# Kernel tuning notes

Measured on AMD Instinct MI355X. Metric: run time of the kernel, lower is better.

The kernel has to match this reference:

```python
import jax, jax.numpy as jnp
import numpy as np

N_NODES = 100000
N_EDGES = 1000000
KEY_DIM = 128
VAL_DIM = 64


def setup_inputs() -> dict:
    key = jax.random.key(0)
    k0, k1, k2, k3, k4, k5 = jax.random.split(key, 6)
    triples = jax.random.randint(k0, (N_EDGES, 3), 0, N_NODES, dtype=jnp.int64)
    ent_feats = jax.random.normal(k1, (N_NODES, KEY_DIM), dtype=jnp.float32)
    att_feats = jax.random.normal(k2, (N_NODES, KEY_DIM), dtype=jnp.float32)
    val_feats = jax.random.normal(k3, (N_NODES, VAL_DIM), dtype=jnp.float32)
    # a: Linear(2*key_dim, 1) -> weight vector [2k], bias [1]
    a_w = jax.random.normal(k4, (2 * KEY_DIM,), dtype=jnp.float32) * (1.0 / np.sqrt(2 * KEY_DIM))
    a_b = jnp.zeros((1,), dtype=jnp.float32)
    W = jax.random.normal(k5, (KEY_DIM + VAL_DIM, KEY_DIM), dtype=jnp.float32) * (1.0 / np.sqrt(KEY_DIM + VAL_DIM))
    return {"attribute_triples": triples, "ent_feats": ent_feats,
            "att_feats": att_feats, "val_feats": val_feats,
            "a_w": a_w, "a_b": a_b, "W": W}


def reference(attribute_triples, ent_feats, att_feats, val_feats, a_w, a_b, W):
    N = ent_feats.shape[0]
    h = attribute_triples[:, 0]
    att = attribute_triples[:, 1]
    val = attribute_triples[:, 2]
    # edge attention score: a([e_h ; a_att]) -> leaky_relu -> exp
    e_h = ent_feats[h]            # [E, K]
    a_f = att_feats[att]          # [E, K]
    score = jnp.concatenate((e_h, a_f), axis=-1) @ a_w + a_b[0]   # [E]
    score = jnp.exp(jax.nn.leaky_relu(score, negative_slope=0.2))
    # segment softmax denominator per head node
    row_sum = jax.ops.segment_sum(score, h, num_segments=N)       # [N]
    attention_p = score / row_sum[h]                               # [E]
    # projected edge messages, weighted by attention, scattered to nodes
    av = jnp.concatenate((a_f, val_feats[val]), axis=-1) @ W       # [E, K]
    av = av * attention_p[:, None]
    to_feats = jax.ops.segment_sum(av, h, num_segments=N)          # [N, K]
    return jax.nn.elu(to_feats + ent_feats)
```

## Files before the change

kernel.cpp:

```cpp
#include <hip/hip_runtime.h>

#define N_NODES 100000
#define N_EDGES 1000000
#define CAP     40

typedef __attribute__((ext_vector_type(4))) float float4_t;
typedef __attribute__((ext_vector_type(2))) _Float16 half2v;
typedef __attribute__((ext_vector_type(4))) _Float16 half4v;
typedef __attribute__((ext_vector_type(8))) _Float16 half8v;
typedef unsigned long long ull;

__device__ __forceinline__ unsigned short f_to_h(float f) {
    union { float f; unsigned int i; } c; c.f = f;
    unsigned int i = c.i;
    unsigned int e = ((i >> 23) & 0xffu) - 112u;
    unsigned int m = i & 0x7fffffu;
    unsigned int r = (e << 10) | (m >> 13);
    r += (m >> 12) & 1u;
    return (unsigned short)r;
}
__device__ __forceinline__ float h_to_f(unsigned short h) {
    union { unsigned int i; float f; } c;
    c.i = (((unsigned int)(h & 0x7fffu)) << 13) + 0x38000000u;
    return c.f;
}
__device__ __forceinline__ unsigned int packh2(float x, float y) {
    half2v h; h.x = (_Float16)x; h.y = (_Float16)y;
    return __builtin_bit_cast(unsigned int, h);
}
__device__ __forceinline__ int clampi(int x) {
    return x < 0 ? 0 : (x >= N_NODES ? N_NODES - 1 : x);
}

__global__ __launch_bounds__(256)
void k_node_scores(const float* __restrict__ ent,
                   const float* __restrict__ attf,
                   const float* __restrict__ valf,
                   const float* __restrict__ aw,
                   float* __restrict__ s_ent, float* __restrict__ s_att,
                   unsigned short* __restrict__ attb,
                   unsigned short* __restrict__ valb) {
    int node = (int)blockIdx.x * 8 + (int)(threadIdx.x >> 5);
    int l32 = threadIdx.x & 31;
    const float4_t* aw4 = (const float4_t*)aw;
    float4_t we4 = aw4[l32];
    float4_t wa4 = aw4[32 + l32];
    float4_t e4 = ((const float4_t*)ent)[(size_t)node * 32 + l32];
    float4_t a4 = ((const float4_t*)attf)[(size_t)node * 32 + l32];
    float2 v2 = ((const float2*)valf)[(size_t)node * 32 + l32];
    if (attb) {
        uint2 pk; pk.x = packh2(a4.x, a4.y); pk.y = packh2(a4.z, a4.w);
        *(uint2*)(attb + (size_t)node * 128 + l32 * 4) = pk;
        ((unsigned int*)valb)[(size_t)node * 32 + l32] = packh2(v2.x, v2.y);
    }
    float se = e4.x * we4.x + e4.y * we4.y + e4.z * we4.z + e4.w * we4.w;
    float sa = a4.x * wa4.x + a4.y * wa4.y + a4.z * wa4.z + a4.w * wa4.w;
#pragma unroll
    for (int off = 16; off >= 1; off >>= 1) {
        se += __shfl_xor(se, off, 64);
        sa += __shfl_xor(sa, off, 64);
    }
    if (l32 == 0) { s_ent[node] = se; s_att[node] = sa; }
}

__global__ __launch_bounds__(256)
void k_prepW(const float* __restrict__ W, unsigned short* __restrict__ Wt) {
    int i = (int)(blockIdx.x * blockDim.x + threadIdx.x);
    if (i >= 192 * 128) return;
    int c = i / 192, k = i - c * 192;
    Wt[i] = __builtin_bit_cast(unsigned short, (_Float16)W[k * 128 + c]);
}

__global__ __launch_bounds__(256)
void k_place(const int* __restrict__ tri,
             const float* __restrict__ s_ent, const float* __restrict__ s_att,
             const float* __restrict__ abp,
             int* __restrict__ cursor, ull* __restrict__ edges) {
    int t = (int)(blockIdx.x * blockDim.x + threadIdx.x);
    if (t >= N_EDGES / 4) return;
    const int4* t4 = (const int4*)tri;
    int4 w0 = t4[3 * t], w1 = t4[3 * t + 1], w2 = t4[3 * t + 2];
    int hs[4] = {w0.x, w0.w, w1.z, w2.y};
    int as[4] = {w0.y, w1.x, w1.w, w2.z};
    int vs[4] = {w0.z, w1.y, w2.x, w2.w};
    float ab = abp[0];
#pragma unroll
    for (int i = 0; i < 4; ++i) {
        int h = clampi(hs[i]), a = clampi(as[i]), v = clampi(vs[i]);
        float s = s_ent[h] + s_att[a] + ab;
        s = s > 0.f ? s : 0.2f * s;
        float sc = __expf(s);
        int slot = atomicAdd(&cursor[h], 1);
        if (slot < CAP) {
            ull pk = (ull)(unsigned)a | ((ull)(unsigned)v << 17) | ((ull)f_to_h(sc) << 34);
            __builtin_nontemporal_store(pk, edges + (size_t)h * CAP + slot);
        }
    }
}

__global__ __launch_bounds__(256)
void k_fused_h(const int* __restrict__ cursor, const ull* __restrict__ edges,
               const unsigned short* __restrict__ attb, const unsigned short* __restrict__ valb,
               const unsigned short* __restrict__ Wt, const float* __restrict__ ent,
               float* __restrict__ out) {
    __shared__ unsigned short Gl[16][200];
    int w = threadIdx.x >> 6, lane = threadIdx.x & 63;
    int grp = lane >> 4, l = lane & 15;
    int base = (int)blockIdx.x * 16;
    int node = base + w * 4 + grp;
    int src = grp << 4;

    int cnt = cursor[node]; cnt = cnt > CAP ? CAP : cnt;
    size_t beg = (size_t)node * CAP;
    const half8v* ap = (const half8v*)attb;
    const half4v* vp = (const half4v*)valb;

    half8v accA = {};
    half4v accV = {};
    float rsum = 0.f;
    int nbat = (cnt + 15) >> 4;
    for (int b = 0; b < nbat; ++b) {
        int idx = b * 16 + l;
        ull edreg = __builtin_nontemporal_load(edges + beg + (idx < cnt ? idx : 0));
        int lim = cnt - b * 16; lim = lim > 16 ? 16 : lim;
#pragma unroll
        for (int c = 0; c < 4; ++c) {
            int j0 = c * 4;
            if (j0 < lim) {
                bool m1 = j0 + 1 < lim, m2 = j0 + 2 < lim, m3 = j0 + 3 < lim;
                ull e0 = __shfl(edreg, src | j0, 64);
                ull e1 = __shfl(edreg, src | (m1 ? j0 + 1 : 0), 64);
                ull e2 = __shfl(edreg, src | (m2 ? j0 + 2 : 0), 64);
                ull e3 = __shfl(edreg, src | (m3 ? j0 + 3 : 0), 64);
                int a0 = (int)(e0 & 0x1FFFFu), v0 = (int)((e0 >> 17) & 0x1FFFFu);
                int a1 = m1 ? (int)(e1 & 0x1FFFFu) : 0, v1 = m1 ? (int)((e1 >> 17) & 0x1FFFFu) : 0;
                int a2 = m2 ? (int)(e2 & 0x1FFFFu) : 0, v2 = m2 ? (int)((e2 >> 17) & 0x1FFFFu) : 0;
                int a3 = m3 ? (int)(e3 & 0x1FFFFu) : 0, v3 = m3 ? (int)((e3 >> 17) & 0x1FFFFu) : 0;
                _Float16 s0 = __builtin_bit_cast(_Float16, (unsigned short)(e0 >> 34));
                _Float16 s1 = m1 ? __builtin_bit_cast(_Float16, (unsigned short)(e1 >> 34)) : (_Float16)0.f;
                _Float16 s2 = m2 ? __builtin_bit_cast(_Float16, (unsigned short)(e2 >> 34)) : (_Float16)0.f;
                _Float16 s3 = m3 ? __builtin_bit_cast(_Float16, (unsigned short)(e3 >> 34)) : (_Float16)0.f;
                half8v A0 = ap[a0 * 16 + l];
                half4v V0 = vp[v0 * 16 + l];
                half8v A1 = ap[a1 * 16 + l];
                half4v V1 = vp[v1 * 16 + l];
                half8v A2 = ap[a2 * 16 + l];
                half4v V2 = vp[v2 * 16 + l];
                half8v A3 = ap[a3 * 16 + l];
                half4v V3 = vp[v3 * 16 + l];
                rsum += (float)s0 + (float)s1 + (float)s2 + (float)s3;
                accA += A0 * s0; accV += V0 * s0;
                accA += A1 * s1; accV += V1 * s1;
                accA += A2 * s2; accV += V2 * s2;
                accA += A3 * s3; accV += V3 * s3;
            }
        }
    }
    {
        float inv = rsum > 0.f ? 1.f / rsum : 0.f;
        _Float16 ih = (_Float16)inv;
        unsigned short* gp = &Gl[w * 4 + grp][0];
        *(half8v*)(gp + l * 8) = accA * ih;
        *(half4v*)(gp + 128 + l * 4) = accV * ih;
    }
    __syncthreads();

    int quad = grp, mn = l;
    float4_t acc0 = {0.f, 0.f, 0.f, 0.f}, acc1 = {0.f, 0.f, 0.f, 0.f};
#pragma unroll
    for (int kt = 0; kt < 6; ++kt) {
        half8v afr = *(const half8v*)(&Gl[mn][quad * 8 + kt * 32]);
        half8v b0 = *(const half8v*)(Wt + (size_t)((w * 2 + 0) * 16 + mn) * 192 + quad * 8 + kt * 32);
        half8v b1 = *(const half8v*)(Wt + (size_t)((w * 2 + 1) * 16 + mn) * 192 + quad * 8 + kt * 32);
        acc0 = __builtin_amdgcn_mfma_f32_16x16x32_f16(afr, b0, acc0, 0, 0, 0);
        acc1 = __builtin_amdgcn_mfma_f32_16x16x32_f16(afr, b1, acc1, 0, 0, 0);
    }
#pragma unroll
    for (int cti = 0; cti < 2; ++cti) {
        float4_t acc = cti ? acc1 : acc0;
        int col = (w * 2 + cti) * 16 + mn;
#pragma unroll
        for (int r = 0; r < 4; ++r) {
            int nd = base + quad * 4 + r;
            float x = acc[r] + __builtin_nontemporal_load(ent + (size_t)nd * 128 + col);
            __builtin_nontemporal_store(x > 0.f ? x : expm1f(x),
                                        out + (size_t)nd * 128 + col);
        }
    }
}

__global__ __launch_bounds__(256)
void k_fused_f32(const int* __restrict__ cursor, const ull* __restrict__ edges,
                 const float* __restrict__ attf, const float* __restrict__ valf,
                 const unsigned short* __restrict__ Wt, const float* __restrict__ ent,
                 float* __restrict__ out) {
    __shared__ unsigned short Gl[16][200];
    int w = threadIdx.x >> 6, lane = threadIdx.x & 63;
    int grp = lane >> 4, l = lane & 15;
    int base = (int)blockIdx.x * 16;

    for (int nn = 0; nn < 4; ++nn) {
        int node = base + w * 4 + nn;
        int cnt = cursor[node]; if (cnt > CAP) cnt = CAP;
        size_t beg = (size_t)node * CAP;
        float aa[8] = {0.f, 0.f, 0.f, 0.f, 0.f, 0.f, 0.f, 0.f};
        float av[4] = {0.f, 0.f, 0.f, 0.f};
        float rsum = 0.f;
        for (int j = grp; j < cnt; j += 4) {
            ull ed = edges[beg + j];
            int a = (int)(ed & 0x1FFFFu);
            int v = (int)((ed >> 17) & 0x1FFFFu);
            float sc = h_to_f((unsigned short)(ed >> 34));
            rsum += sc;
            const float4_t* ap = (const float4_t*)(attf + (size_t)a * 128);
            float4_t f0 = ap[l], f1 = ap[16 + l];
            float4_t fv = ((const float4_t*)(valf + (size_t)v * 64))[l];
#pragma unroll
            for (int q = 0; q < 4; ++q) {
                aa[q] += sc * f0[q]; aa[4 + q] += sc * f1[q]; av[q] += sc * fv[q];
            }
        }
#pragma unroll
        for (int q = 0; q < 8; ++q) {
            aa[q] += __shfl_xor(aa[q], 16, 64);
            aa[q] += __shfl_xor(aa[q], 32, 64);
        }
#pragma unroll
        for (int q = 0; q < 4; ++q) {
            av[q] += __shfl_xor(av[q], 16, 64);
            av[q] += __shfl_xor(av[q], 32, 64);
        }
        rsum += __shfl_xor(rsum, 16, 64);
        rsum += __shfl_xor(rsum, 32, 64);
        if (grp == 0) {
            float inv = rsum > 0.f ? 1.f / rsum : 0.f;
            unsigned short* gp = &Gl[w * 4 + nn][0];
            uint2 p0; p0.x = packh2(aa[0] * inv, aa[1] * inv); p0.y = packh2(aa[2] * inv, aa[3] * inv);
            *(uint2*)(gp + l * 4) = p0;
            uint2 p1; p1.x = packh2(aa[4] * inv, aa[5] * inv); p1.y = packh2(aa[6] * inv, aa[7] * inv);
            *(uint2*)(gp + 64 + l * 4) = p1;
            uint2 pv; pv.x = packh2(av[0] * inv, av[1] * inv); pv.y = packh2(av[2] * inv, av[3] * inv);
            *(uint2*)(gp + 128 + l * 4) = pv;
        }
    }
    __syncthreads();

    int quad = grp, mn = l;
    float4_t acc0 = {0.f, 0.f, 0.f, 0.f}, acc1 = {0.f, 0.f, 0.f, 0.f};
#pragma unroll
    for (int kt = 0; kt < 6; ++kt) {
        half8v afr = *(const half8v*)(&Gl[mn][quad * 8 + kt * 32]);
        half8v b0 = *(const half8v*)(Wt + (size_t)((w * 2 + 0) * 16 + mn) * 192 + quad * 8 + kt * 32);
        half8v b1 = *(const half8v*)(Wt + (size_t)((w * 2 + 1) * 16 + mn) * 192 + quad * 8 + kt * 32);
        acc0 = __builtin_amdgcn_mfma_f32_16x16x32_f16(afr, b0, acc0, 0, 0, 0);
        acc1 = __builtin_amdgcn_mfma_f32_16x16x32_f16(afr, b1, acc1, 0, 0, 0);
    }
#pragma unroll
    for (int cti = 0; cti < 2; ++cti) {
        float4_t acc = cti ? acc1 : acc0;
        int col = (w * 2 + cti) * 16 + mn;
#pragma unroll
        for (int r = 0; r < 4; ++r) {
            int node = base + quad * 4 + r;
            float x = acc[r] + ent[(size_t)node * 128 + col];
            out[(size_t)node * 128 + col] = x > 0.f ? x : expm1f(x);
        }
    }
}

extern "C" void kernel_launch(void* const* d_in, const int* in_sizes, int n_in,
                              void* d_out, int out_size, void* d_ws, size_t ws_size,
                              hipStream_t stream) {
    const int*   tri  = (const int*)d_in[0];
    const float* ent  = (const float*)d_in[1];
    const float* attf = (const float*)d_in[2];
    const float* valf = (const float*)d_in[3];
    const float* aw   = (const float*)d_in[4];
    const float* ab   = (const float*)d_in[5];
    const float* W    = (const float*)d_in[6];
    float* out = (float*)d_out;

    char* ws = (char*)d_ws;
    size_t off = 0;
    int*   cursor = (int*)(ws + off);   off += (size_t)N_NODES * 4;
    float* s_ent  = (float*)(ws + off); off += (size_t)N_NODES * 4;
    float* s_att  = (float*)(ws + off); off += (size_t)N_NODES * 4;
    unsigned short* Wt = (unsigned short*)(ws + off); off += 192 * 128 * 2;
    ull* edges = (ull*)(ws + off);      off += (size_t)N_NODES * CAP * 8;
    unsigned short* attb = (unsigned short*)(ws + off); off += (size_t)N_NODES * 128 * 2;
    unsigned short* valb = (unsigned short*)(ws + off); off += (size_t)N_NODES * 64 * 2;
    size_t need = off;
    int h16 = ws_size >= need;

    hipMemsetAsync(cursor, 0, (size_t)N_NODES * 4, stream);

    k_node_scores<<<N_NODES / 8, 256, 0, stream>>>(ent, attf, valf, aw, s_ent, s_att,
                                                   h16 ? attb : (unsigned short*)nullptr,
                                                   h16 ? valb : (unsigned short*)nullptr);
    k_prepW<<<(192 * 128 + 255) / 256, 256, 0, stream>>>(W, Wt);
    k_place<<<(N_EDGES / 4 + 255) / 256, 256, 0, stream>>>(tri, s_ent, s_att, ab, cursor, edges);
    if (h16)
        k_fused_h<<<N_NODES / 16, 256, 0, stream>>>(cursor, edges, attb, valb, Wt, ent, out);
    else
        k_fused_f32<<<N_NODES / 16, 256, 0, stream>>>(cursor, edges, attf, valf, Wt, ent, out);
}
```

Before: 328.4 us.

## Fuse all stages into one persistent kernel with grid barriers and dynamic tile scheduling

Replaces the memset plus four kernel launches with a single persistent kernel sized to full occupancy. Software grid barriers separate the node-score, edge-placement and gather/MFMA phases, and an atomic tile counter hands out work in the final phase. This is meant to remove launch gaps and tail effects between stages. In exchange, the grid barriers add spin-wait cost, the persistent grid may reduce latency hiding in the memory-bound phases, and the edge loop now reads the triples with scalar loads instead of int4 loads.

```diff
diff --git a/kernel.cpp b/kernel.cpp
--- a/kernel.cpp
+++ b/kernel.cpp
@@ -3,6 +3,7 @@
 #define N_NODES 100000
 #define N_EDGES 1000000
 #define CAP     40
+#define NTILES  (N_NODES / 16)
 
 typedef __attribute__((ext_vector_type(4))) float float4_t;
 typedef __attribute__((ext_vector_type(2))) _Float16 half2v;
@@ -32,14 +33,183 @@
     return x < 0 ? 0 : (x >= N_NODES ? N_NODES - 1 : x);
 }
 
+__device__ __forceinline__ void grid_barrier(int* cnt, int nblocks) {
+    __syncthreads();
+    if (threadIdx.x == 0) {
+        __threadfence();
+        __hip_atomic_fetch_add(cnt, 1, __ATOMIC_ACQ_REL, __HIP_MEMORY_SCOPE_AGENT);
+        while (__hip_atomic_load(cnt, __ATOMIC_ACQUIRE, __HIP_MEMORY_SCOPE_AGENT) < nblocks)
+            __builtin_amdgcn_s_sleep(2);
+    }
+    __syncthreads();
+}
+
+__global__ __launch_bounds__(256, 8)
+void k_mega(const int* __restrict__ tri, const float* __restrict__ ent,
+            const float* __restrict__ attf, const float* __restrict__ valf,
+            const float* __restrict__ aw, const float* __restrict__ abp,
+            const float* __restrict__ W,
+            int* __restrict__ ctrl,
+            int* __restrict__ cursor, float* __restrict__ s_ent, float* __restrict__ s_att,
+            unsigned short* __restrict__ attb, unsigned short* __restrict__ valb,
+            unsigned short* __restrict__ Wt, ull* __restrict__ edges,
+            float* __restrict__ out) {
+    int tid = threadIdx.x;
+    int gtid = (int)blockIdx.x * 256 + tid;
+    int gsz = (int)gridDim.x * 256;
+    int l32 = tid & 31;
+
+    for (int i = gtid; i < N_NODES; i += gsz) cursor[i] = 0;
+    for (int i = gtid; i < 192 * 128; i += gsz) {
+        int c = i / 192, k = i - c * 192;
+        Wt[i] = __builtin_bit_cast(unsigned short, (_Float16)W[k * 128 + c]);
+    }
+    {
+        const float4_t* aw4 = (const float4_t*)aw;
+        float4_t we4 = aw4[l32];
+        float4_t wa4 = aw4[32 + l32];
+        int halfid = ((int)blockIdx.x << 3) + (tid >> 5);
+        int nstep = (int)gridDim.x << 3;
+        for (int node = halfid; node < N_NODES; node += nstep) {
+            float4_t e4 = ((const float4_t*)ent)[(size_t)node * 32 + l32];
+            float4_t a4 = ((const float4_t*)attf)[(size_t)node * 32 + l32];
+            float se = e4.x * we4.x + e4.y * we4.y + e4.z * we4.z + e4.w * we4.w;
+            float sa = a4.x * wa4.x + a4.y * wa4.y + a4.z * wa4.z + a4.w * wa4.w;
+#pragma unroll
+            for (int off = 16; off >= 1; off >>= 1) {
+                se += __shfl_xor(se, off, 64);
+                sa += __shfl_xor(sa, off, 64);
+            }
+            if (l32 == 0) { s_ent[node] = se; s_att[node] = sa; }
+        }
+    }
+    grid_barrier(&ctrl[0], (int)gridDim.x);
+
+    {
+        int halfid = ((int)blockIdx.x << 3) + (tid >> 5);
+        int nstep = (int)gridDim.x << 3;
+        for (int node = halfid; node < N_NODES; node += nstep) {
+            float4_t a4 = ((const float4_t*)attf)[(size_t)node * 32 + l32];
+            float2 v2 = ((const float2*)valf)[(size_t)node * 32 + l32];
+            uint2 pk; pk.x = packh2(a4.x, a4.y); pk.y = packh2(a4.z, a4.w);
+            *(uint2*)(attb + (size_t)node * 128 + l32 * 4) = pk;
+            ((unsigned int*)valb)[(size_t)node * 32 + l32] = packh2(v2.x, v2.y);
+        }
+        float ab = abp[0];
+        for (int e = gtid; e < N_EDGES; e += gsz) {
+            int h = clampi(tri[3 * e]);
+            int a = clampi(tri[3 * e + 1]);
+            int v = clampi(tri[3 * e + 2]);
+            float s = s_ent[h] + s_att[a] + ab;
+            s = s > 0.f ? s : 0.2f * s;
+            float sc = __expf(s);
+            int slot = atomicAdd(&cursor[h], 1);
+            if (slot < CAP) {
+                ull pk = (ull)(unsigned)a | ((ull)(unsigned)v << 17) | ((ull)f_to_h(sc) << 34);
+                __builtin_nontemporal_store(pk, edges + (size_t)h * CAP + slot);
+            }
+        }
+    }
+    grid_barrier(&ctrl[1], (int)gridDim.x);
+
+    __shared__ unsigned short Gl[16][200];
+    __shared__ int s_tile;
+    int w = tid >> 6, lane = tid & 63;
+    int grp = lane >> 4, l = lane & 15;
+    const half8v* ap = (const half8v*)attb;
+    const half4v* vp = (const half4v*)valb;
+    for (;;) {
+        __syncthreads();
+        if (tid == 0) s_tile = atomicAdd(&ctrl[2], 1);
+        __syncthreads();
+        int tile = s_tile;
+        if (tile >= NTILES) break;
+        int base = tile * 16;
+        int node = base + w * 4 + grp;
+        int src = grp << 4;
+        int cnt = cursor[node]; cnt = cnt > CAP ? CAP : cnt;
+        size_t beg = (size_t)node * CAP;
+
+        half8v accA = {};
+        half4v accV = {};
+        float rsum = 0.f;
+        int nbat = (cnt + 15) >> 4;
+        for (int b = 0; b < nbat; ++b) {
+            int idx = b * 16 + l;
+            ull edreg = __builtin_nontemporal_load(edges + beg + (idx < cnt ? idx : 0));
+            int lim = cnt - b * 16; lim = lim > 16 ? 16 : lim;
+#pragma unroll
+            for (int c = 0; c < 4; ++c) {
+                int j0 = c * 4;
+                if (j0 < lim) {
+                    bool m1 = j0 + 1 < lim, m2 = j0 + 2 < lim, m3 = j0 + 3 < lim;
+                    ull e0 = __shfl(edreg, src | j0, 64);
+                    ull e1 = __shfl(edreg, src | (m1 ? j0 + 1 : 0), 64);
+                    ull e2 = __shfl(edreg, src | (m2 ? j0 + 2 : 0), 64);
+                    ull e3 = __shfl(edreg, src | (m3 ? j0 + 3 : 0), 64);
+                    int a0 = (int)(e0 & 0x1FFFFu), v0 = (int)((e0 >> 17) & 0x1FFFFu);
+                    int a1 = m1 ? (int)(e1 & 0x1FFFFu) : 0, v1 = m1 ? (int)((e1 >> 17) & 0x1FFFFu) : 0;
+                    int a2 = m2 ? (int)(e2 & 0x1FFFFu) : 0, v2 = m2 ? (int)((e2 >> 17) & 0x1FFFFu) : 0;
+                    int a3 = m3 ? (int)(e3 & 0x1FFFFu) : 0, v3 = m3 ? (int)((e3 >> 17) & 0x1FFFFu) : 0;
+                    _Float16 s0 = __builtin_bit_cast(_Float16, (unsigned short)(e0 >> 34));
+                    _Float16 s1 = m1 ? __builtin_bit_cast(_Float16, (unsigned short)(e1 >> 34)) : (_Float16)0.f;
+                    _Float16 s2 = m2 ? __builtin_bit_cast(_Float16, (unsigned short)(e2 >> 34)) : (_Float16)0.f;
+                    _Float16 s3 = m3 ? __builtin_bit_cast(_Float16, (unsigned short)(e3 >> 34)) : (_Float16)0.f;
+                    half8v A0 = ap[a0 * 16 + l];
+                    half4v V0 = vp[v0 * 16 + l];
+                    half8v A1 = ap[a1 * 16 + l];
+                    half4v V1 = vp[v1 * 16 + l];
+                    half8v A2 = ap[a2 * 16 + l];
+                    half4v V2 = vp[v2 * 16 + l];
+                    half8v A3 = ap[a3 * 16 + l];
+                    half4v V3 = vp[v3 * 16 + l];
+                    rsum += (float)s0 + (float)s1 + (float)s2 + (float)s3;
+                    accA += A0 * s0; accV += V0 * s0;
+                    accA += A1 * s1; accV += V1 * s1;
+                    accA += A2 * s2; accV += V2 * s2;
+                    accA += A3 * s3; accV += V3 * s3;
+                }
+            }
+        }
+        {
+            float inv = rsum > 0.f ? 1.f / rsum : 0.f;
+            _Float16 ih = (_Float16)inv;
+            unsigned short* gp = &Gl[w * 4 + grp][0];
+            *(half8v*)(gp + l * 8) = accA * ih;
+            *(half4v*)(gp + 128 + l * 4) = accV * ih;
+        }
+        __syncthreads();
+
+        int quad = grp, mn = l;
+        float4_t acc0 = {0.f, 0.f, 0.f, 0.f}, acc1 = {0.f, 0.f, 0.f, 0.f};
+#pragma unroll
+        for (int kt = 0; kt < 6; ++kt) {
+            half8v afr = *(const half8v*)(&Gl[mn][quad * 8 + kt * 32]);
+            half8v b0 = *(const half8v*)(Wt + (size_t)((w * 2 + 0) * 16 + mn) * 192 + quad * 8 + kt * 32);
+            half8v b1 = *(const half8v*)(Wt + (size_t)((w * 2 + 1) * 16 + mn) * 192 + quad * 8 + kt * 32);
+            acc0 = __builtin_amdgcn_mfma_f32_16x16x32_f16(afr, b0, acc0, 0, 0, 0);
+            acc1 = __builtin_amdgcn_mfma_f32_16x16x32_f16(afr, b1, acc1, 0, 0, 0);
+        }
+#pragma unroll
+        for (int cti = 0; cti < 2; ++cti) {
+            float4_t acc = cti ? acc1 : acc0;
+            int col = (w * 2 + cti) * 16 + mn;
+#pragma unroll
+            for (int r = 0; r < 4; ++r) {
+                int nd = base + quad * 4 + r;
+                float x = acc[r] + __builtin_nontemporal_load(ent + (size_t)nd * 128 + col);
+                __builtin_nontemporal_store(x > 0.f ? x : expm1f(x),
+                                            out + (size_t)nd * 128 + col);
+            }
+        }
+    }
+}
+
 __global__ __launch_bounds__(256)
-void k_node_scores(const float* __restrict__ ent,
-                   const float* __restrict__ attf,
-                   const float* __restrict__ valf,
-                   const float* __restrict__ aw,
+void k_node_scores(const float* __restrict__ ent, const float* __restrict__ attf,
+                   const float* __restrict__ valf, const float* __restrict__ aw,
                    float* __restrict__ s_ent, float* __restrict__ s_att,
-                   unsigned short* __restrict__ attb,
-                   unsigned short* __restrict__ valb) {
+                   unsigned short* __restrict__ attb, unsigned short* __restrict__ valb) {
     int node = (int)blockIdx.x * 8 + (int)(threadIdx.x >> 5);
     int l32 = threadIdx.x & 31;
     const float4_t* aw4 = (const float4_t*)aw;
@@ -72,120 +242,21 @@
 }
 
 __global__ __launch_bounds__(256)
-void k_place(const int* __restrict__ tri,
-             const float* __restrict__ s_ent, const float* __restrict__ s_att,
-             const float* __restrict__ abp,
+void k_place(const int* __restrict__ tri, const float* __restrict__ s_ent,
+             const float* __restrict__ s_att, const float* __restrict__ abp,
              int* __restrict__ cursor, ull* __restrict__ edges) {
-    int t = (int)(blockIdx.x * blockDim.x + threadIdx.x);
-    if (t >= N_EDGES / 4) return;
-    const int4* t4 = (const int4*)tri;
-    int4 w0 = t4[3 * t], w1 = t4[3 * t + 1], w2 = t4[3 * t + 2];
-    int hs[4] = {w0.x, w0.w, w1.z, w2.y};
-    int as[4] = {w0.y, w1.x, w1.w, w2.z};
-    int vs[4] = {w0.z, w1.y, w2.x, w2.w};
-    float ab = abp[0];
-#pragma unroll
-    for (int i = 0; i < 4; ++i) {
-        int h = clampi(hs[i]), a = clampi(as[i]), v = clampi(vs[i]);
-        float s = s_ent[h] + s_att[a] + ab;
-        s = s > 0.f ? s : 0.2f * s;
-        float sc = __expf(s);
-        int slot = atomicAdd(&cursor[h], 1);
-        if (slot < CAP) {
-            ull pk = (ull)(unsigned)a | ((ull)(unsigned)v << 17) | ((ull)f_to_h(sc) << 34);
-            __builtin_nontemporal_store(pk, edges + (size_t)h * CAP + slot);
-        }
-    }
-}
-
-__global__ __launch_bounds__(256)
-void k_fused_h(const int* __restrict__ cursor, const ull* __restrict__ edges,
-               const unsigned short* __restrict__ attb, const unsigned short* __restrict__ valb,
-               const unsigned short* __restrict__ Wt, const float* __restrict__ ent,
-               float* __restrict__ out) {
-    __shared__ unsigned short Gl[16][200];
-    int w = threadIdx.x >> 6, lane = threadIdx.x & 63;
-    int grp = lane >> 4, l = lane & 15;
-    int base = (int)blockIdx.x * 16;
-    int node = base + w * 4 + grp;
-    int src = grp << 4;
-
-    int cnt = cursor[node]; cnt = cnt > CAP ? CAP : cnt;
-    size_t beg = (size_t)node * CAP;
-    const half8v* ap = (const half8v*)attb;
-    const half4v* vp = (const half4v*)valb;
-
-    half8v accA = {};
-    half4v accV = {};
-    float rsum = 0.f;
-    int nbat = (cnt + 15) >> 4;
-    for (int b = 0; b < nbat; ++b) {
-        int idx = b * 16 + l;
-        ull edreg = __builtin_nontemporal_load(edges + beg + (idx < cnt ? idx : 0));
-        int lim = cnt - b * 16; lim = lim > 16 ? 16 : lim;
-#pragma unroll
-        for (int c = 0; c < 4; ++c) {
-            int j0 = c * 4;
-            if (j0 < lim) {
-                bool m1 = j0 + 1 < lim, m2 = j0 + 2 < lim, m3 = j0 + 3 < lim;
-                ull e0 = __shfl(edreg, src | j0, 64);
-                ull e1 = __shfl(edreg, src | (m1 ? j0 + 1 : 0), 64);
-                ull e2 = __shfl(edreg, src | (m2 ? j0 + 2 : 0), 64);
-                ull e3 = __shfl(edreg, src | (m3 ? j0 + 3 : 0), 64);
-                int a0 = (int)(e0 & 0x1FFFFu), v0 = (int)((e0 >> 17) & 0x1FFFFu);
-                int a1 = m1 ? (int)(e1 & 0x1FFFFu) : 0, v1 = m1 ? (int)((e1 >> 17) & 0x1FFFFu) : 0;
-                int a2 = m2 ? (int)(e2 & 0x1FFFFu) : 0, v2 = m2 ? (int)((e2 >> 17) & 0x1FFFFu) : 0;
-                int a3 = m3 ? (int)(e3 & 0x1FFFFu) : 0, v3 = m3 ? (int)((e3 >> 17) & 0x1FFFFu) : 0;
-                _Float16 s0 = __builtin_bit_cast(_Float16, (unsigned short)(e0 >> 34));
-                _Float16 s1 = m1 ? __builtin_bit_cast(_Float16, (unsigned short)(e1 >> 34)) : (_Float16)0.f;
-                _Float16 s2 = m2 ? __builtin_bit_cast(_Float16, (unsigned short)(e2 >> 34)) : (_Float16)0.f;
-                _Float16 s3 = m3 ? __builtin_bit_cast(_Float16, (unsigned short)(e3 >> 34)) : (_Float16)0.f;
-                half8v A0 = ap[a0 * 16 + l];
-                half4v V0 = vp[v0 * 16 + l];
-                half8v A1 = ap[a1 * 16 + l];
-                half4v V1 = vp[v1 * 16 + l];
-                half8v A2 = ap[a2 * 16 + l];
-                half4v V2 = vp[v2 * 16 + l];
-                half8v A3 = ap[a3 * 16 + l];
-                half4v V3 = vp[v3 * 16 + l];
-                rsum += (float)s0 + (float)s1 + (float)s2 + (float)s3;
-                accA += A0 * s0; accV += V0 * s0;
-                accA += A1 * s1; accV += V1 * s1;
-                accA += A2 * s2; accV += V2 * s2;
-                accA += A3 * s3; accV += V3 * s3;
-            }
-        }
-    }
-    {
-        float inv = rsum > 0.f ? 1.f / rsum : 0.f;
-        _Float16 ih = (_Float16)inv;
-        unsigned short* gp = &Gl[w * 4 + grp][0];
-        *(half8v*)(gp + l * 8) = accA * ih;
-        *(half4v*)(gp + 128 + l * 4) = accV * ih;
-    }
-    __syncthreads();
-
-    int quad = grp, mn = l;
-    float4_t acc0 = {0.f, 0.f, 0.f, 0.f}, acc1 = {0.f, 0.f, 0.f, 0.f};
-#pragma unroll
-    for (int kt = 0; kt < 6; ++kt) {
-        half8v afr = *(const half8v*)(&Gl[mn][quad * 8 + kt * 32]);
-        half8v b0 = *(const half8v*)(Wt + (size_t)((w * 2 + 0) * 16 + mn) * 192 + quad * 8 + kt * 32);
-        half8v b1 = *(const half8v*)(Wt + (size_t)((w * 2 + 1) * 16 + mn) * 192 + quad * 8 + kt * 32);
-        acc0 = __builtin_amdgcn_mfma_f32_16x16x32_f16(afr, b0, acc0, 0, 0, 0);
-        acc1 = __builtin_amdgcn_mfma_f32_16x16x32_f16(afr, b1, acc1, 0, 0, 0);
-    }
-#pragma unroll
-    for (int cti = 0; cti < 2; ++cti) {
-        float4_t acc = cti ? acc1 : acc0;
-        int col = (w * 2 + cti) * 16 + mn;
-#pragma unroll
-        for (int r = 0; r < 4; ++r) {
-            int nd = base + quad * 4 + r;
-            float x = acc[r] + __builtin_nontemporal_load(ent + (size_t)nd * 128 + col);
-            __builtin_nontemporal_store(x > 0.f ? x : expm1f(x),
-                                        out + (size_t)nd * 128 + col);
-        }
+    int e = (int)(blockIdx.x * blockDim.x + threadIdx.x);
+    if (e >= N_EDGES) return;
+    int h = clampi(tri[3 * e]);
+    int a = clampi(tri[3 * e + 1]);
+    int v = clampi(tri[3 * e + 2]);
+    float s = s_ent[h] + s_att[a] + abp[0];
+    s = s > 0.f ? s : 0.2f * s;
+    float sc = __expf(s);
+    int slot = atomicAdd(&cursor[h], 1);
+    if (slot < CAP) {
+        ull pk = (ull)(unsigned)a | ((ull)(unsigned)v << 17) | ((ull)f_to_h(sc) << 34);
+        __builtin_nontemporal_store(pk, edges + (size_t)h * CAP + slot);
     }
 }
 
@@ -198,7 +269,6 @@
     int w = threadIdx.x >> 6, lane = threadIdx.x & 63;
     int grp = lane >> 4, l = lane & 15;
     int base = (int)blockIdx.x * 16;
-
     for (int nn = 0; nn < 4; ++nn) {
         int node = base + w * 4 + nn;
         int cnt = cursor[node]; if (cnt > CAP) cnt = CAP;
@@ -244,7 +314,6 @@
         }
     }
     __syncthreads();
-
     int quad = grp, mn = l;
     float4_t acc0 = {0.f, 0.f, 0.f, 0.f}, acc1 = {0.f, 0.f, 0.f, 0.f};
 #pragma unroll
@@ -282,6 +351,7 @@
 
     char* ws = (char*)d_ws;
     size_t off = 0;
+    int*   ctrl   = (int*)(ws + off);   off += 256;
     int*   cursor = (int*)(ws + off);   off += (size_t)N_NODES * 4;
     float* s_ent  = (float*)(ws + off); off += (size_t)N_NODES * 4;
     float* s_att  = (float*)(ws + off); off += (size_t)N_NODES * 4;
@@ -292,15 +362,30 @@
     size_t need = off;
     int h16 = ws_size >= need;
 
-    hipMemsetAsync(cursor, 0, (size_t)N_NODES * 4, stream);
-
-    k_node_scores<<<N_NODES / 8, 256, 0, stream>>>(ent, attf, valf, aw, s_ent, s_att,
-                                                   h16 ? attb : (unsigned short*)nullptr,
-                                                   h16 ? valb : (unsigned short*)nullptr);
-    k_prepW<<<(192 * 128 + 255) / 256, 256, 0, stream>>>(W, Wt);
-    k_place<<<(N_EDGES / 4 + 255) / 256, 256, 0, stream>>>(tri, s_ent, s_att, ab, cursor, edges);
-    if (h16)
-        k_fused_h<<<N_NODES / 16, 256, 0, stream>>>(cursor, edges, attb, valb, Wt, ent, out);
-    else
+    static int s_nb = 0;
+    if (s_nb == 0) {
+        int occ = 0, ncu = 0, dev = 0;
+        if (hipOccupancyMaxActiveBlocksPerMultiprocessor(&occ, k_mega, 256, 0) != hipSuccess || occ <= 0)
+            occ = -1;
+        (void)hipGetDevice(&dev);
+        if (hipDeviceGetAttribute(&ncu, hipDeviceAttributeMultiprocessorCount, dev) != hipSuccess || ncu <= 0)
+            ncu = 256;
+        s_nb = (occ > 0) ? occ * ncu : -1;
+        if (s_nb > 4096) s_nb = 4096;
+    }
+
+    if (h16 && s_nb > 0) {
+        (void)hipMemsetAsync(ctrl, 0, 12, stream);
+        k_mega<<<s_nb, 256, 0, stream>>>(tri, ent, attf, valf, aw, ab, W,
+                                         ctrl, cursor, s_ent, s_att,
+                                         attb, valb, Wt, edges, out);
+    } else {
+        (void)hipMemsetAsync(cursor, 0, (size_t)N_NODES * 4, stream);
+        k_node_scores<<<N_NODES / 8, 256, 0, stream>>>(ent, attf, valf, aw, s_ent, s_att,
+                                                       h16 ? attb : (unsigned short*)nullptr,
+                                                       h16 ? valb : (unsigned short*)nullptr);
+        k_prepW<<<(192 * 128 + 255) / 256, 256, 0, stream>>>(W, Wt);
+        k_place<<<(N_EDGES + 255) / 256, 256, 0, stream>>>(tri, s_ent, s_att, ab, cursor, edges);
         k_fused_f32<<<N_NODES / 16, 256, 0, stream>>>(cursor, edges, attf, valf, Wt, ent, out);
-}
+    }
+}
```

After: 617.0 us. 87.9% more time.

## Merge node-score prep and edge bucketing into one concurrent kernel, compute scores in gather

Applied to the files above, without the earlier changes.

Edge placement no longer depends on node scores: bucketing stores only (att,val) indices, and the fused gather kernel recomputes each edge's attention score from s_ent[node]+s_att[a]. That lets node-score/fp16 conversion, W transpose and edge bucketing run in one persistent kernel, with even and odd blocks doing the two jobs in opposite order so they overlap. Two launches and a dependency barrier go away. The cost is an extra s_att gather plus an exp per edge in the gather kernel, and the fallback path is refactored into separate kernels.

```diff
diff --git a/kernel.cpp b/kernel.cpp
--- a/kernel.cpp
+++ b/kernel.cpp
@@ -3,6 +3,7 @@
 #define N_NODES 100000
 #define N_EDGES 1000000
 #define CAP     40
+#define NPREP   2048
 
 typedef __attribute__((ext_vector_type(4))) float float4_t;
 typedef __attribute__((ext_vector_type(2))) _Float16 half2v;
@@ -33,73 +34,69 @@
 }
 
 __global__ __launch_bounds__(256)
-void k_node_scores(const float* __restrict__ ent,
-                   const float* __restrict__ attf,
-                   const float* __restrict__ valf,
-                   const float* __restrict__ aw,
-                   float* __restrict__ s_ent, float* __restrict__ s_att,
-                   unsigned short* __restrict__ attb,
-                   unsigned short* __restrict__ valb) {
-    int node = (int)blockIdx.x * 8 + (int)(threadIdx.x >> 5);
-    int l32 = threadIdx.x & 31;
-    const float4_t* aw4 = (const float4_t*)aw;
-    float4_t we4 = aw4[l32];
-    float4_t wa4 = aw4[32 + l32];
-    float4_t e4 = ((const float4_t*)ent)[(size_t)node * 32 + l32];
-    float4_t a4 = ((const float4_t*)attf)[(size_t)node * 32 + l32];
-    float2 v2 = ((const float2*)valf)[(size_t)node * 32 + l32];
-    if (attb) {
-        uint2 pk; pk.x = packh2(a4.x, a4.y); pk.y = packh2(a4.z, a4.w);
-        *(uint2*)(attb + (size_t)node * 128 + l32 * 4) = pk;
-        ((unsigned int*)valb)[(size_t)node * 32 + l32] = packh2(v2.x, v2.y);
-    }
-    float se = e4.x * we4.x + e4.y * we4.y + e4.z * we4.z + e4.w * we4.w;
-    float sa = a4.x * wa4.x + a4.y * wa4.y + a4.z * wa4.z + a4.w * wa4.w;
-#pragma unroll
-    for (int off = 16; off >= 1; off >>= 1) {
-        se += __shfl_xor(se, off, 64);
-        sa += __shfl_xor(sa, off, 64);
-    }
-    if (l32 == 0) { s_ent[node] = se; s_att[node] = sa; }
-}
-
-__global__ __launch_bounds__(256)
-void k_prepW(const float* __restrict__ W, unsigned short* __restrict__ Wt) {
-    int i = (int)(blockIdx.x * blockDim.x + threadIdx.x);
-    if (i >= 192 * 128) return;
-    int c = i / 192, k = i - c * 192;
-    Wt[i] = __builtin_bit_cast(unsigned short, (_Float16)W[k * 128 + c]);
-}
-
-__global__ __launch_bounds__(256)
-void k_place(const int* __restrict__ tri,
-             const float* __restrict__ s_ent, const float* __restrict__ s_att,
-             const float* __restrict__ abp,
-             int* __restrict__ cursor, ull* __restrict__ edges) {
-    int t = (int)(blockIdx.x * blockDim.x + threadIdx.x);
-    if (t >= N_EDGES / 4) return;
-    const int4* t4 = (const int4*)tri;
-    int4 w0 = t4[3 * t], w1 = t4[3 * t + 1], w2 = t4[3 * t + 2];
-    int hs[4] = {w0.x, w0.w, w1.z, w2.y};
-    int as[4] = {w0.y, w1.x, w1.w, w2.z};
-    int vs[4] = {w0.z, w1.y, w2.x, w2.w};
-    float ab = abp[0];
-#pragma unroll
-    for (int i = 0; i < 4; ++i) {
-        int h = clampi(hs[i]), a = clampi(as[i]), v = clampi(vs[i]);
-        float s = s_ent[h] + s_att[a] + ab;
-        s = s > 0.f ? s : 0.2f * s;
-        float sc = __expf(s);
-        int slot = atomicAdd(&cursor[h], 1);
-        if (slot < CAP) {
-            ull pk = (ull)(unsigned)a | ((ull)(unsigned)v << 17) | ((ull)f_to_h(sc) << 34);
-            __builtin_nontemporal_store(pk, edges + (size_t)h * CAP + slot);
+void k_prep(const int* __restrict__ tri, const float* __restrict__ ent,
+            const float* __restrict__ attf, const float* __restrict__ valf,
+            const float* __restrict__ aw, const float* __restrict__ W,
+            float* __restrict__ s_ent, float* __restrict__ s_att,
+            unsigned short* __restrict__ attb, unsigned short* __restrict__ valb,
+            unsigned short* __restrict__ Wt,
+            int* __restrict__ cursor, ull* __restrict__ edges) {
+    int bid = (int)blockIdx.x, nbk = (int)gridDim.x, tid = threadIdx.x;
+    bool even = (bid & 1) == 0;
+#pragma unroll
+    for (int pass = 0; pass < 2; ++pass) {
+        if ((pass == 0) == even) {
+            int l32 = tid & 31;
+            const float4_t* aw4 = (const float4_t*)aw;
+            float4_t we4 = aw4[l32];
+            float4_t wa4 = aw4[32 + l32];
+            int halfid = bid * 8 + (tid >> 5);
+            int nstep = nbk * 8;
+            for (int node = halfid; node < N_NODES; node += nstep) {
+                float4_t e4 = ((const float4_t*)ent)[(size_t)node * 32 + l32];
+                float4_t a4 = ((const float4_t*)attf)[(size_t)node * 32 + l32];
+                float2 v2 = ((const float2*)valf)[(size_t)node * 32 + l32];
+                uint2 pk; pk.x = packh2(a4.x, a4.y); pk.y = packh2(a4.z, a4.w);
+                *(uint2*)(attb + (size_t)node * 128 + l32 * 4) = pk;
+                ((unsigned int*)valb)[(size_t)node * 32 + l32] = packh2(v2.x, v2.y);
+                float se = e4.x * we4.x + e4.y * we4.y + e4.z * we4.z + e4.w * we4.w;
+                float sa = a4.x * wa4.x + a4.y * wa4.y + a4.z * wa4.z + a4.w * wa4.w;
+#pragma unroll
+                for (int off = 16; off >= 1; off >>= 1) {
+                    se += __shfl_xor(se, off, 64);
+                    sa += __shfl_xor(sa, off, 64);
+                }
+                if (l32 == 0) { s_ent[node] = se; s_att[node] = sa; }
+            }
+            for (int i = bid * 256 + tid; i < 192 * 128; i += nbk * 256) {
+                int c = i / 192, k = i - c * 192;
+                Wt[i] = __builtin_bit_cast(unsigned short, (_Float16)W[k * 128 + c]);
+            }
+        } else {
+            const int4* t4 = (const int4*)tri;
+            for (int t = bid * 256 + tid; t < N_EDGES / 4; t += nbk * 256) {
+                int4 w0 = t4[3 * t], w1 = t4[3 * t + 1], w2 = t4[3 * t + 2];
+                int hs[4] = {w0.x, w0.w, w1.z, w2.y};
+                int as[4] = {w0.y, w1.x, w1.w, w2.z};
+                int vs[4] = {w0.z, w1.y, w2.x, w2.w};
+#pragma unroll
+                for (int i = 0; i < 4; ++i) {
+                    int h = clampi(hs[i]), a = clampi(as[i]), v = clampi(vs[i]);
+                    int slot = atomicAdd(&cursor[h], 1);
+                    if (slot < CAP) {
+                        ull pk = (ull)(unsigned)a | ((ull)(unsigned)v << 17);
+                        __builtin_nontemporal_store(pk, edges + (size_t)h * CAP + slot);
+                    }
+                }
+            }
         }
     }
 }
 
 __global__ __launch_bounds__(256)
 void k_fused_h(const int* __restrict__ cursor, const ull* __restrict__ edges,
+               const float* __restrict__ s_ent, const float* __restrict__ s_att,
+               const float* __restrict__ abp,
                const unsigned short* __restrict__ attb, const unsigned short* __restrict__ valb,
                const unsigned short* __restrict__ Wt, const float* __restrict__ ent,
                float* __restrict__ out) {
@@ -114,6 +111,7 @@
     size_t beg = (size_t)node * CAP;
     const half8v* ap = (const half8v*)attb;
     const half4v* vp = (const half4v*)valb;
+    float seh = s_ent[node] + abp[0];
 
     half8v accA = {};
     half4v accV = {};
@@ -136,10 +134,7 @@
                 int a1 = m1 ? (int)(e1 & 0x1FFFFu) : 0, v1 = m1 ? (int)((e1 >> 17) & 0x1FFFFu) : 0;
                 int a2 = m2 ? (int)(e2 & 0x1FFFFu) : 0, v2 = m2 ? (int)((e2 >> 17) & 0x1FFFFu) : 0;
                 int a3 = m3 ? (int)(e3 & 0x1FFFFu) : 0, v3 = m3 ? (int)((e3 >> 17) & 0x1FFFFu) : 0;
-                _Float16 s0 = __builtin_bit_cast(_Float16, (unsigned short)(e0 >> 34));
-                _Float16 s1 = m1 ? __builtin_bit_cast(_Float16, (unsigned short)(e1 >> 34)) : (_Float16)0.f;
-                _Float16 s2 = m2 ? __builtin_bit_cast(_Float16, (unsigned short)(e2 >> 34)) : (_Float16)0.f;
-                _Float16 s3 = m3 ? __builtin_bit_cast(_Float16, (unsigned short)(e3 >> 34)) : (_Float16)0.f;
+                float t0 = s_att[a0], t1 = s_att[a1], t2 = s_att[a2], t3 = s_att[a3];
                 half8v A0 = ap[a0 * 16 + l];
                 half4v V0 = vp[v0 * 16 + l];
                 half8v A1 = ap[a1 * 16 + l];
@@ -148,6 +143,16 @@
                 half4v V2 = vp[v2 * 16 + l];
                 half8v A3 = ap[a3 * 16 + l];
                 half4v V3 = vp[v3 * 16 + l];
+                float f0 = seh + t0; f0 = f0 > 0.f ? f0 : 0.2f * f0;
+                float f1 = seh + t1; f1 = f1 > 0.f ? f1 : 0.2f * f1;
+                float f2 = seh + t2; f2 = f2 > 0.f ? f2 : 0.2f * f2;
+                float f3 = seh + t3; f3 = f3 > 0.f ? f3 : 0.2f * f3;
+                float sc0 = __expf(f0);
+                float sc1 = m1 ? __expf(f1) : 0.f;
+                float sc2 = m2 ? __expf(f2) : 0.f;
+                float sc3 = m3 ? __expf(f3) : 0.f;
+                _Float16 s0 = (_Float16)sc0, s1 = (_Float16)sc1;
+                _Float16 s2 = (_Float16)sc2, s3 = (_Float16)sc3;
                 rsum += (float)s0 + (float)s1 + (float)s2 + (float)s3;
                 accA += A0 * s0; accV += V0 * s0;
                 accA += A1 * s1; accV += V1 * s1;
@@ -186,6 +191,54 @@
             __builtin_nontemporal_store(x > 0.f ? x : expm1f(x),
                                         out + (size_t)nd * 128 + col);
         }
+    }
+}
+
+__global__ __launch_bounds__(256)
+void k_node_scores(const float* __restrict__ ent, const float* __restrict__ attf,
+                   const float* __restrict__ valf, const float* __restrict__ aw,
+                   float* __restrict__ s_ent, float* __restrict__ s_att) {
+    int node = (int)blockIdx.x * 8 + (int)(threadIdx.x >> 5);
+    int l32 = threadIdx.x & 31;
+    const float4_t* aw4 = (const float4_t*)aw;
+    float4_t we4 = aw4[l32];
+    float4_t wa4 = aw4[32 + l32];
+    float4_t e4 = ((const float4_t*)ent)[(size_t)node * 32 + l32];
+    float4_t a4 = ((const float4_t*)attf)[(size_t)node * 32 + l32];
+    float se = e4.x * we4.x + e4.y * we4.y + e4.z * we4.z + e4.w * we4.w;
+    float sa = a4.x * wa4.x + a4.y * wa4.y + a4.z * wa4.z + a4.w * wa4.w;
+#pragma unroll
+    for (int off = 16; off >= 1; off >>= 1) {
+        se += __shfl_xor(se, off, 64);
+        sa += __shfl_xor(sa, off, 64);
+    }
+    if (l32 == 0) { s_ent[node] = se; s_att[node] = sa; }
+}
+
+__global__ __launch_bounds__(256)
+void k_prepW(const float* __restrict__ W, unsigned short* __restrict__ Wt) {
+    int i = (int)(blockIdx.x * blockDim.x + threadIdx.x);
+    if (i >= 192 * 128) return;
+    int c = i / 192, k = i - c * 192;
+    Wt[i] = __builtin_bit_cast(unsigned short, (_Float16)W[k * 128 + c]);
+}
+
+__global__ __launch_bounds__(256)
+void k_place_sc(const int* __restrict__ tri, const float* __restrict__ s_ent,
+                const float* __restrict__ s_att, const float* __restrict__ abp,
+                int* __restrict__ cursor, ull* __restrict__ edges) {
+    int e = (int)(blockIdx.x * blockDim.x + threadIdx.x);
+    if (e >= N_EDGES) return;
+    int h = clampi(tri[3 * e]);
+    int a = clampi(tri[3 * e + 1]);
+    int v = clampi(tri[3 * e + 2]);
+    float s = s_ent[h] + s_att[a] + abp[0];
+    s = s > 0.f ? s : 0.2f * s;
+    float sc = __expf(s);
+    int slot = atomicAdd(&cursor[h], 1);
+    if (slot < CAP) {
+        ull pk = (ull)(unsigned)a | ((ull)(unsigned)v << 17) | ((ull)f_to_h(sc) << 34);
+        __builtin_nontemporal_store(pk, edges + (size_t)h * CAP + slot);
     }
 }
 
@@ -198,7 +251,6 @@
     int w = threadIdx.x >> 6, lane = threadIdx.x & 63;
     int grp = lane >> 4, l = lane & 15;
     int base = (int)blockIdx.x * 16;
-
     for (int nn = 0; nn < 4; ++nn) {
         int node = base + w * 4 + nn;
         int cnt = cursor[node]; if (cnt > CAP) cnt = CAP;
@@ -244,7 +296,6 @@
         }
     }
     __syncthreads();
-
     int quad = grp, mn = l;
     float4_t acc0 = {0.f, 0.f, 0.f, 0.f}, acc1 = {0.f, 0.f, 0.f, 0.f};
 #pragma unroll
@@ -292,15 +343,17 @@
     size_t need = off;
     int h16 = ws_size >= need;
 
-    hipMemsetAsync(cursor, 0, (size_t)N_NODES * 4, stream);
-
-    k_node_scores<<<N_NODES / 8, 256, 0, stream>>>(ent, attf, valf, aw, s_ent, s_att,
-                                                   h16 ? attb : (unsigned short*)nullptr,
-                                                   h16 ? valb : (unsigned short*)nullptr);
-    k_prepW<<<(192 * 128 + 255) / 256, 256, 0, stream>>>(W, Wt);
-    k_place<<<(N_EDGES / 4 + 255) / 256, 256, 0, stream>>>(tri, s_ent, s_att, ab, cursor, edges);
-    if (h16)
-        k_fused_h<<<N_NODES / 16, 256, 0, stream>>>(cursor, edges, attb, valb, Wt, ent, out);
-    else
+    (void)hipMemsetAsync(cursor, 0, (size_t)N_NODES * 4, stream);
+
+    if (h16) {
+        k_prep<<<NPREP, 256, 0, stream>>>(tri, ent, attf, valf, aw, W,
+                                          s_ent, s_att, attb, valb, Wt, cursor, edges);
+        k_fused_h<<<N_NODES / 16, 256, 0, stream>>>(cursor, edges, s_ent, s_att, ab,
+                                                    attb, valb, Wt, ent, out);
+    } else {
+        k_node_scores<<<N_NODES / 8, 256, 0, stream>>>(ent, attf, valf, aw, s_ent, s_att);
+        k_prepW<<<(192 * 128 + 255) / 256, 256, 0, stream>>>(W, Wt);
+        k_place_sc<<<(N_EDGES + 255) / 256, 256, 0, stream>>>(tri, s_ent, s_att, ab, cursor, edges);
         k_fused_f32<<<N_NODES / 16, 256, 0, stream>>>(cursor, edges, attf, valf, Wt, ent, out);
-}
+    }
+}
```

Result: no change. 323.3 us (-1.6%).
